# Kernel optimization log

Hardware: AMD Instinct MI355X
Metric: run time of the kernel (lower is better)

Reference implementation:

```python
import jax, jax.numpy as jnp
import numpy as np

B, LQ, LC, LN, D, H = 4, 1024, 1024, 1024, 1024, 16
HD = D // H
LS_INIT = 1e-4
RES_MAX = 10.0
EPS = 1e-5


def layernorm(x, g, b):
    mu = jnp.mean(x, axis=-1, keepdims=True)
    var = jnp.var(x, axis=-1, keepdims=True)
    return (x - mu) * jax.lax.rsqrt(var + EPS) * g + b


def setup_inputs() -> dict:
    key = jax.random.key(0)
    ks = jax.random.split(key, 12)
    s = 0.02
    return {
        "tight_tokens": jax.random.normal(ks[0], (B, LQ, D), jnp.float32),
        "context_tokens": jax.random.normal(ks[1], (B, LC, D), jnp.float32),
        "neighborhood_tokens": jax.random.normal(ks[2], (B, LN, D), jnp.float32),
        "ln_q_g": jnp.ones((D,), jnp.float32), "ln_q_b": jnp.zeros((D,), jnp.float32),
        "ln_kv_g": jnp.ones((D,), jnp.float32), "ln_kv_b": jnp.zeros((D,), jnp.float32),
        "in_proj_w": jax.random.normal(ks[3], (3 * D, D), jnp.float32) * s,
        "in_proj_b": jnp.zeros((3 * D,), jnp.float32),
        "out_proj_w": jax.random.normal(ks[4], (D, D), jnp.float32) * s,
        "out_proj_b": jnp.zeros((D,), jnp.float32),
        "cross_gamma": jnp.full((D,), LS_INIT, jnp.float32),
        "ln_f_g": jnp.ones((D,), jnp.float32), "ln_f_b": jnp.zeros((D,), jnp.float32),
        "w1": jax.random.normal(ks[5], (4 * D, D), jnp.float32) * s,
        "b1": jnp.zeros((4 * D,), jnp.float32),
        "w2": jax.random.normal(ks[6], (D, 4 * D), jnp.float32) * s,
        "b2": jnp.zeros((D,), jnp.float32),
        "ffn_gamma": jnp.full((D,), LS_INIT, jnp.float32),
    }


def reference(tight_tokens, context_tokens, neighborhood_tokens,
              ln_q_g, ln_q_b, ln_kv_g, ln_kv_b,
              in_proj_w, in_proj_b, out_proj_w, out_proj_b, cross_gamma,
              ln_f_g, ln_f_b, w1, b1, w2, b2, ffn_gamma):
    kv = jnp.concatenate([context_tokens, neighborhood_tokens], axis=1)  # [B, LKV, D]
    q_in = layernorm(tight_tokens, ln_q_g, ln_q_b)
    kv_in = layernorm(kv, ln_kv_g, ln_kv_b)

    wq, wk, wv = jnp.split(in_proj_w, 3, axis=0)
    bq, bk, bv = jnp.split(in_proj_b, 3, axis=0)
    q = (q_in @ wq.T + bq).reshape(B, LQ, H, HD)
    k = (kv_in @ wk.T + bk).reshape(B, -1, H, HD)
    v = (kv_in @ wv.T + bv).reshape(B, -1, H, HD)

    scores = jnp.einsum('bqhd,bkhd->bhqk', q, k) / jnp.sqrt(jnp.float32(HD))
    attn = jax.nn.softmax(scores, axis=-1)  # [B, H, LQ, LKV]
    ctx = jnp.einsum('bhqk,bkhd->bqhd', attn, v).reshape(B, LQ, D)
    attn_out = ctx @ out_proj_w.T + out_proj_b

    cg = jnp.clip(cross_gamma, -RES_MAX, RES_MAX)
    x = tight_tokens + attn_out * cg

    h = layernorm(x, ln_f_g, ln_f_b)
    h = jax.nn.gelu(h @ w1.T + b1, approximate=False) @ w2.T + b2
    fg = jnp.clip(ffn_gamma, -RES_MAX, RES_MAX)
    x = x + h * fg

    return x, attn.mean(axis=1)
```

## Files before the change

### kernel.cpp

```cpp
#include <hip/hip_runtime.h>
#include <math.h>

typedef unsigned short u16;
typedef __attribute__((ext_vector_type(8))) short bf16x8;
typedef __attribute__((ext_vector_type(4))) float f32x4;

#define MFMA16(a,b,c) __builtin_amdgcn_mfma_f32_16x16x32_bf16(a,b,c,0,0,0)

__device__ __forceinline__ u16 f2bf(float f){
  union { float f; unsigned int u; } x; x.f = f;
  unsigned int r = x.u + 0x7fffu + ((x.u >> 16) & 1u);
  return (u16)(r >> 16);
}

__device__ __forceinline__ void gload16(const void* g, void* lds){
  __builtin_amdgcn_global_load_lds(
    (const __attribute__((address_space(1))) unsigned int*)g,
    (__attribute__((address_space(3))) unsigned int*)lds, 16, 0, 0);
}

__global__ __launch_bounds__(256) void cvt_weights(
    const float* __restrict__ wqkv, const float* __restrict__ wo,
    const float* __restrict__ w1, const float* __restrict__ w2,
    u16* __restrict__ o0, u16* __restrict__ o1,
    u16* __restrict__ o2, u16* __restrict__ o3)
{
  int idx = blockIdx.x * 256 + threadIdx.x;
  const float* src; u16* dst;
  if (idx < 786432)                    { src = wqkv; dst = o0; }
  else if ((idx -= 786432) < 262144)   { src = wo;   dst = o1; }
  else if ((idx -= 262144) < 1048576)  { src = w1;   dst = o2; }
  else { idx -= 1048576;                 src = w2;   dst = o3; }
  float4 v = ((const float4*)src)[idx];
  short4 o;
  o.x = (short)f2bf(v.x); o.y = (short)f2bf(v.y);
  o.z = (short)f2bf(v.z); o.w = (short)f2bf(v.w);
  ((short4*)dst)[idx] = o;
}

template<int MODE>
__global__ __launch_bounds__(256) void ln_kernel(
    const float* __restrict__ s0, const float* __restrict__ s1,
    const float* __restrict__ g, const float* __restrict__ be,
    u16* __restrict__ out)
{
  int row = blockIdx.x, t = threadIdx.x;
  const float* src;
  if (MODE == 1) {
    int b = row >> 11, p = row & 2047;
    src = (p < 1024) ? s0 + ((long)(b*1024 + p))*1024
                     : s1 + ((long)(b*1024 + p - 1024))*1024;
  } else {
    src = s0 + (long)row * 1024;
  }
  float4 v = ((const float4*)src)[t];
  float s  = v.x + v.y + v.z + v.w;
  float ss = v.x*v.x + v.y*v.y + v.z*v.z + v.w*v.w;
  #pragma unroll
  for (int m = 1; m < 64; m <<= 1) { s += __shfl_xor(s, m); ss += __shfl_xor(ss, m); }
  __shared__ float red[8];
  int l = t & 63, w = t >> 6;
  if (l == 0) { red[w*2] = s; red[w*2+1] = ss; }
  __syncthreads();
  s  = red[0] + red[2] + red[4] + red[6];
  ss = red[1] + red[3] + red[5] + red[7];
  float mean = s * (1.0f/1024.0f);
  float var  = ss * (1.0f/1024.0f) - mean*mean;
  float rstd = rsqrtf(var + 1e-5f);
  float4 gv = ((const float4*)g)[t];
  float4 bv = ((const float4*)be)[t];
  short4 o;
  o.x = (short)f2bf((v.x-mean)*rstd*gv.x + bv.x);
  o.y = (short)f2bf((v.y-mean)*rstd*gv.y + bv.y);
  o.z = (short)f2bf((v.z-mean)*rstd*gv.z + bv.z);
  o.w = (short)f2bf((v.w-mean)*rstd*gv.w + bv.w);
  *(short4*)(out + (long)row*1024 + t*4) = o;
}

template<int EPI, int BM>
__global__ __launch_bounds__(256,2) void gemm_bt(
    const u16* __restrict__ A, const u16* __restrict__ Bt,
    int M, int N, int K,
    const float* __restrict__ bias,
    const float* __restrict__ gamma,
    const float* __restrict__ resid,
    float* __restrict__ outf,
    u16* __restrict__ outb0, u16* __restrict__ outb1)
{
  constexpr int MI = BM / 32;
  __shared__ __align__(16) u16 at[2][BM*64];
  __shared__ __align__(16) u16 bt[2][128*64];
  int nwg = gridDim.x;
  int bidx = (blockIdx.x & 7) * (nwg >> 3) + (blockIdx.x >> 3);
  int nb = N >> 7;
  int tm = bidx / nb, tn = bidx % nb;
  int m0 = tm * BM, n0 = tn << 7;
  int t = threadIdx.x, l = t & 63, w = t >> 6;
  int wr = (w >> 1) * (BM/2), wc = (w & 1) * 64;
  int fr = l & 15, fq = l >> 4;
  f32x4 acc[MI][4] = {};
  int rr = t >> 3;
  int cb = (t & 7) << 4;
  const char* Ab = (const char*)A;
  const char* Bp = (const char*)Bt;
  long ld = (long)K * 2;

#define G_STAGE(s, kt) do {                                                        \
    _Pragma("unroll")                                                              \
    for (int c = 0; c < MI; c++) {                                                 \
      int row = c*32 + rr;                                                         \
      gload16(Ab + (long)(m0 + row)*ld + (long)(kt)*2 + (cb ^ ((row & 7) << 4)),   \
              (char*)at[s] + c*4096 + w*1024);                                     \
    }                                                                              \
    _Pragma("unroll")                                                              \
    for (int c = 0; c < 4; c++) {                                                  \
      int row = c*32 + rr;                                                         \
      gload16(Bp + (long)(n0 + row)*ld + (long)(kt)*2 + (cb ^ ((row & 7) << 4)),   \
              (char*)bt[s] + c*4096 + w*1024);                                     \
    }                                                                              \
  } while (0)

  G_STAGE(0, 0);
  __syncthreads();
  int cur = 0;
  for (int kt = 0; kt < K; kt += 64) {
    if (kt + 64 < K) G_STAGE(cur ^ 1, kt + 64);
    #pragma unroll
    for (int ka = 0; ka < 2; ka++) {
      bf16x8 af[MI], bfv[4];
      #pragma unroll
      for (int i = 0; i < MI; i++) {
        int ra = wr + i*16 + fr;
        af[i] = *(const bf16x8*)((const char*)at[cur] + ra*128 + ((ka*64 + fq*16) ^ ((ra & 7) << 4)));
      }
      #pragma unroll
      for (int j = 0; j < 4; j++) {
        int rb = wc + j*16 + fr;
        bfv[j] = *(const bf16x8*)((const char*)bt[cur] + rb*128 + ((ka*64 + fq*16) ^ ((rb & 7) << 4)));
      }
      #pragma unroll
      for (int i = 0; i < MI; i++)
        #pragma unroll
        for (int j = 0; j < 4; j++)
          acc[i][j] = MFMA16(af[i], bfv[j], acc[i][j]);
    }
    __syncthreads();
    cur ^= 1;
  }
#undef G_STAGE
  #pragma unroll
  for (int i = 0; i < MI; i++) {
    #pragma unroll
    for (int j = 0; j < 4; j++) {
      #pragma unroll
      for (int r = 0; r < 4; r++) {
        int row = m0 + wr + i*16 + fq*4 + r;
        int col = n0 + wc + j*16 + fr;
        float v = acc[i][j][r];
        if constexpr (EPI == 0) {
          float qv = (v + bias[col]) * 0.18033688011112042f;
          int b = row >> 10, lq = row & 1023, h = col >> 6, hd = col & 63;
          outb0[(((long)(b*16 + h)) << 16) + (lq << 6) + hd] = f2bf(qv);
        } else if constexpr (EPI == 1) {
          float u = v + bias[col];
          int b = row >> 11, p = row & 2047;
          if (col < 1024) {
            int h = col >> 6, hd = col & 63;
            outb0[(((long)((b*16 + h)*2048 + p)) << 6) + hd] = f2bf(u);
          } else {
            int c2 = col - 1024, h = c2 >> 6, hd = c2 & 63;
            outb1[(((long)((b*16 + h)*64 + hd)) << 11) + p] = f2bf(u);
          }
        } else if constexpr (EPI == 2) {
          float gs = gamma[col]; gs = fminf(fmaxf(gs, -10.f), 10.f);
          long idx = (long)row*1024 + col;
          outf[idx] = resid[idx] + (v + bias[col]) * gs;
        } else if constexpr (EPI == 3) {
          float u = v + bias[col];
          float ge = 0.5f * u * (1.0f + erff(u * 0.70710678118654752f));
          outb0[(long)row*4096 + col] = f2bf(ge);
        } else {
          float gs = gamma[col]; gs = fminf(fmaxf(gs, -10.f), 10.f);
          long idx = (long)row*1024 + col;
          outf[idx] = resid[idx] + (v + bias[col]) * gs;
        }
      }
    }
  }
}

__global__ __launch_bounds__(256, 3) void flash_fwd(
    const u16* __restrict__ q, const u16* __restrict__ k,
    const u16* __restrict__ vt, u16* __restrict__ ctx,
    float* __restrict__ ilout)
{
  __shared__ __align__(16) u16 ks[2][64*64];
  __shared__ __align__(16) u16 vs[2][64*64];
  __shared__ __align__(16) char ps[4*4096];
  int nwg = gridDim.x;
  int bid = (blockIdx.x & 7) * (nwg >> 3) + (blockIdx.x >> 3);
  int qt = bid & 7, h = (bid >> 3) & 15, b = bid >> 7;
  int q0 = qt << 7;
  int t = threadIdx.x, l = t & 63, w = t >> 6;
  int fr = l & 15, fq = l >> 4;
  const char* qb = (const char*)(q  + (((long)(b*16 + h)) << 16));
  const char* kb = (const char*)(k  + (((long)(b*16 + h)) << 17));
  const char* vb = (const char*)(vt + (((long)(b*16 + h)) << 17));
  char* psw = ps + w*4096;
  int rr = t >> 3;
  int sc = (t & 7) << 4;

  #pragma unroll
  for (int c = 0; c < 2; c++) {
    int row = c*32 + rr;
    gload16(kb + (long)row*128 + (sc ^ ((row & 7) << 4)), (char*)ks[0] + c*4096 + w*1024);
    gload16(vb + (long)row*4096 + (sc ^ ((row & 7) << 4)), (char*)vs[0] + c*4096 + w*1024);
  }
  {
    int qr = l >> 3;
    #pragma unroll
    for (int c = 0; c < 4; c++) {
      int row = c*8 + qr;
      gload16(qb + (long)(q0 + w*32 + row)*128 + (sc ^ ((row & 7) << 4)), psw + c*1024);
    }
  }
  asm volatile("s_waitcnt vmcnt(0)" ::: "memory");
  bf16x8 qf[2][2];
  #pragma unroll
  for (int rf = 0; rf < 2; rf++) {
    int row = rf*16 + fr;
    qf[rf][0] = *(const bf16x8*)(psw + row*128 + ((fq*16) ^ ((row & 7) << 4)));
    qf[rf][1] = *(const bf16x8*)(psw + row*128 + ((64 + fq*16) ^ ((row & 7) << 4)));
  }
  asm volatile("s_waitcnt lgkmcnt(0)" ::: "memory");
  __builtin_amdgcn_s_barrier();
  asm volatile("" ::: "memory");

  f32x4 cacc[2][4] = {};
  f32x4 lrun[2] = {{0.f,0.f,0.f,0.f},{0.f,0.f,0.f,0.f}};
  int cur = 0;
  for (int kt = 0; kt < 2048; kt += 64) {
    int notlast = (kt + 64 < 2048);
    if (notlast) {
      #pragma unroll
      for (int c = 0; c < 2; c++) {
        int row = c*32 + rr;
        gload16(vb + (long)row*4096 + (long)(kt + 64)*2 + (sc ^ ((row & 7) << 4)),
                (char*)vs[cur ^ 1] + c*4096 + w*1024);
        gload16(kb + (long)(kt + 64 + row)*128 + (sc ^ ((row & 7) << 4)),
                (char*)ks[cur ^ 1] + c*4096 + w*1024);
      }
    }
    __builtin_amdgcn_sched_barrier(0);
    const char* ksb = (const char*)ks[cur];
    f32x4 sf[2][4];
    __builtin_amdgcn_s_setprio(1);
    #pragma unroll
    for (int cf = 0; cf < 4; cf++) {
      int row = cf*16 + fr;
      bf16x8 kf0 = *(const bf16x8*)(ksb + row*128 + ((fq*16) ^ ((row & 7) << 4)));
      bf16x8 kf1 = *(const bf16x8*)(ksb + row*128 + ((64 + fq*16) ^ ((row & 7) << 4)));
      #pragma unroll
      for (int rf = 0; rf < 2; rf++) {
        f32x4 a = {};
        a = MFMA16(qf[rf][0], kf0, a);
        sf[rf][cf] = MFMA16(qf[rf][1], kf1, a);
      }
    }
    __builtin_amdgcn_s_setprio(0);
    #pragma unroll
    for (int rf = 0; rf < 2; rf++)
      #pragma unroll
      for (int cf = 0; cf < 4; cf++)
        #pragma unroll
        for (int r = 0; r < 4; r++) {
          float pv = exp2f(sf[rf][cf][r]);
          lrun[rf][r] += pv;
          union { float f; unsigned int u; } pu; pu.f = pv;
          int prow = rf*16 + fq*4 + r;
          *(u16*)(psw + prow*128 + (((cf*16 + fr) << 1) ^ ((prow & 7) << 4))) = (u16)(pu.u >> 16);
        }
    bf16x8 pa[2][2];
    #pragma unroll
    for (int rf = 0; rf < 2; rf++) {
      int row = rf*16 + fr;
      pa[rf][0] = *(const bf16x8*)(psw + row*128 + ((fq*16) ^ ((row & 7) << 4)));
      pa[rf][1] = *(const bf16x8*)(psw + row*128 + ((64 + fq*16) ^ ((row & 7) << 4)));
    }
    __builtin_amdgcn_s_setprio(1);
    #pragma unroll
    for (int cfd = 0; cfd < 4; cfd++) {
      int hd = cfd*16 + fr;
      bf16x8 vf0 = *(const bf16x8*)((const char*)vs[cur] + hd*128 + ((fq*16) ^ ((hd & 7) << 4)));
      bf16x8 vf1 = *(const bf16x8*)((const char*)vs[cur] + hd*128 + ((64 + fq*16) ^ ((hd & 7) << 4)));
      #pragma unroll
      for (int rf = 0; rf < 2; rf++) {
        cacc[rf][cfd] = MFMA16(pa[rf][0], vf0, cacc[rf][cfd]);
        cacc[rf][cfd] = MFMA16(pa[rf][1], vf1, cacc[rf][cfd]);
      }
    }
    __builtin_amdgcn_s_setprio(0);
    if (notlast) {
      asm volatile("s_waitcnt vmcnt(0)" ::: "memory");
      __builtin_amdgcn_s_barrier();
      asm volatile("" ::: "memory");
    }
    cur ^= 1;
  }
  #pragma unroll
  for (int rf = 0; rf < 2; rf++) {
    float il4[4];
    #pragma unroll
    for (int r = 0; r < 4; r++) {
      float s = lrun[rf][r];
      #pragma unroll
      for (int msk = 1; msk < 16; msk <<= 1) s += __shfl_xor(s, msk, 16);
      il4[r] = 1.0f / s;
    }
    #pragma unroll
    for (int cf = 0; cf < 4; cf++)
      #pragma unroll
      for (int r = 0; r < 4; r++) {
        int row = q0 + w*32 + rf*16 + fq*4 + r;
        int col = h*64 + cf*16 + fr;
        ctx[(long)(b*1024 + row)*1024 + col] = f2bf(cacc[rf][cf][r] * il4[r]);
      }
    if (fr == 0) {
      #pragma unroll
      for (int r = 0; r < 4; r++) {
        int row = q0 + w*32 + rf*16 + fq*4 + r;
        long idx = (((long)(b*16 + h)) << 10) + row;
        ilout[idx] = il4[r];
      }
    }
  }
}

__global__ __launch_bounds__(256,2) void attn_mean(
    const u16* __restrict__ q, const u16* __restrict__ k,
    const float* __restrict__ il,
    float* __restrict__ out)
{
  __shared__ __align__(16) u16 qs[2][128*64];
  __shared__ __align__(16) u16 ks[2][128*64];
  __shared__ __align__(16) float ml[2][128];
  int nwg = gridDim.x;
  int bid = (blockIdx.x & 7) * (nwg >> 3) + (blockIdx.x >> 3);
  int kt = bid & 15, qt = (bid >> 4) & 7, b = bid >> 7;
  int q0 = qt << 7, k0 = kt << 7;
  int t = threadIdx.x, l = t & 63, w = t >> 6;
  int wr = (w >> 1) << 6, wc = (w & 1) << 6;
  int fr = l & 15, fq = l >> 4;
  int rr = t >> 3, cbb = (t & 7) << 4;
  const long bh = (long)b * 16;

#define AM_STAGE(hh, s) do {                                                        \
    const char* qb_ = (const char*)(q + ((bh + (hh)) << 16)) + (long)q0*128;        \
    const char* kb_ = (const char*)(k + ((bh + (hh)) << 17)) + (long)k0*128;        \
    _Pragma("unroll")                                                               \
    for (int c = 0; c < 4; c++) {                                                   \
      int row = c*32 + rr;                                                          \
      int sw = cbb ^ ((row & 7) << 4);                                              \
      gload16(qb_ + (long)row*128 + sw, (char*)qs[s] + c*4096 + w*1024);            \
      gload16(kb_ + (long)row*128 + sw, (char*)ks[s] + c*4096 + w*1024);            \
    }                                                                               \
    if (w == 0 && l < 32) {                                                         \
      gload16((const char*)(il + ((bh + (hh)) << 10) + q0) + l*16, (char*)ml[s]);   \
    }                                                                               \
  } while (0)

  AM_STAGE(0, 0);
  asm volatile("s_waitcnt vmcnt(0)" ::: "memory");
  __builtin_amdgcn_s_barrier();
  asm volatile("" ::: "memory");

  f32x4 macc[4][4] = {};
  for (int h = 0; h < 16; h++) {
    int cur = h & 1;
    if (h < 15) AM_STAGE(h + 1, cur ^ 1);
    const char* qsb = (const char*)qs[cur];
    const char* ksb = (const char*)ks[cur];
    const float* mlb = ml[cur];
    f32x4 ir4[4];
    #pragma unroll
    for (int i = 0; i < 4; i++)
      ir4[i] = *(const f32x4*)(mlb + wr + i*16 + fq*4);
    bf16x8 af[4][2], bf[4][2];
    #pragma unroll
    for (int i = 0; i < 4; i++) {
      int ra = wr + i*16 + fr;
      int rb = wc + i*16 + fr;
      af[i][0] = *(const bf16x8*)(qsb + ra*128 + ((fq*16) ^ ((ra & 7) << 4)));
      af[i][1] = *(const bf16x8*)(qsb + ra*128 + ((64 + fq*16) ^ ((ra & 7) << 4)));
      bf[i][0] = *(const bf16x8*)(ksb + rb*128 + ((fq*16) ^ ((rb & 7) << 4)));
      bf[i][1] = *(const bf16x8*)(ksb + rb*128 + ((64 + fq*16) ^ ((rb & 7) << 4)));
    }
    #pragma unroll
    for (int j = 0; j < 4; j++) {
      f32x4 sf[4];
      __builtin_amdgcn_s_setprio(1);
      #pragma unroll
      for (int i = 0; i < 4; i++) {
        f32x4 a = MFMA16(af[i][0], bf[j][0], {});
        sf[i] = MFMA16(af[i][1], bf[j][1], a);
      }
      __builtin_amdgcn_s_setprio(0);
      #pragma unroll
      for (int i = 0; i < 4; i++)
        #pragma unroll
        for (int r = 0; r < 4; r++)
          macc[i][j][r] += exp2f(sf[i][r]) * ir4[i][r];
    }
    asm volatile("s_waitcnt vmcnt(0)" ::: "memory");
    __builtin_amdgcn_s_barrier();
    asm volatile("" ::: "memory");
  }
#undef AM_STAGE
  #pragma unroll
  for (int i = 0; i < 4; i++)
    #pragma unroll
    for (int j = 0; j < 4; j++)
      #pragma unroll
      for (int r = 0; r < 4; r++) {
        int row = q0 + wr + i*16 + fq*4 + r;
        int col = k0 + wc + j*16 + fr;
        out[((long)(b*1024 + row) << 11) + col] = macc[i][j][r] * 0.0625f;
      }
}

extern "C" void kernel_launch(void* const* d_in, const int* in_sizes, int n_in,
                              void* d_out, int out_size, void* d_ws, size_t ws_size,
                              hipStream_t stream)
{
  (void)in_sizes; (void)n_in; (void)out_size; (void)ws_size;
  const float* tight = (const float*)d_in[0];
  const float* ctxt  = (const float*)d_in[1];
  const float* nbh   = (const float*)d_in[2];
  const float* lnqg  = (const float*)d_in[3];
  const float* lnqb  = (const float*)d_in[4];
  const float* lnkg  = (const float*)d_in[5];
  const float* lnkb  = (const float*)d_in[6];
  const float* wqkv  = (const float*)d_in[7];
  const float* bqkv  = (const float*)d_in[8];
  const float* wo    = (const float*)d_in[9];
  const float* bo    = (const float*)d_in[10];
  const float* cg    = (const float*)d_in[11];
  const float* lnfg  = (const float*)d_in[12];
  const float* lnfb  = (const float*)d_in[13];
  const float* w1    = (const float*)d_in[14];
  const float* b1    = (const float*)d_in[15];
  const float* w2    = (const float*)d_in[16];
  const float* b2    = (const float*)d_in[17];
  const float* fg    = (const float*)d_in[18];

  char* p = (char*)d_ws;
  u16* wqkv_bf = (u16*)p; p += 3072L*1024*2;
  u16* wo_bf   = (u16*)p; p += 1024L*1024*2;
  u16* w1_bf   = (u16*)p; p += 4096L*1024*2;
  u16* w2_bf   = (u16*)p; p += 1024L*4096*2;
  u16* qin_bf  = (u16*)p; p += 4096L*1024*2;
  u16* kvin_bf = (u16*)p; p += 8192L*1024*2;
  u16* q_bf    = (u16*)p; p += 4L*16*1024*64*2;
  u16* k_bf    = (u16*)p; p += 4L*16*2048*64*2;
  u16* vt_bf   = (u16*)p; p += 4L*16*64*2048*2;
  u16* ctx_bf  = (u16*)p; p += 4096L*1024*2;
  float* il_f  = (float*)p; p += 4L*16*1024*4;
  float* x_f   = (float*)p; p += 4096L*1024*4;
  u16* hln_bf  = (u16*)p; p += 4096L*1024*2;
  u16* gelu_bf = (u16*)p; p += 4096L*4096*2;

  float* x_out    = (float*)d_out;
  float* mean_out = x_out + 4194304;

  cvt_weights<<<12288, 256, 0, stream>>>(wqkv, wo, w1, w2, wqkv_bf, wo_bf, w1_bf, w2_bf);
  ln_kernel<0><<<4096, 256, 0, stream>>>(tight, nullptr, lnqg, lnqb, qin_bf);
  ln_kernel<1><<<8192, 256, 0, stream>>>(ctxt, nbh, lnkg, lnkb, kvin_bf);
  gemm_bt<0,64><<<512, 256, 0, stream>>>(qin_bf, wqkv_bf, 4096, 1024, 1024,
                                      bqkv, nullptr, nullptr, nullptr, q_bf, nullptr);
  gemm_bt<1,128><<<1024, 256, 0, stream>>>(kvin_bf, wqkv_bf + 1024L*1024, 8192, 2048, 1024,
                                       bqkv + 1024, nullptr, nullptr, nullptr, k_bf, vt_bf);
  flash_fwd<<<512, 256, 0, stream>>>(q_bf, k_bf, vt_bf, ctx_bf, il_f);
  attn_mean<<<512, 256, 0, stream>>>(q_bf, k_bf, il_f, mean_out);
  gemm_bt<2,64><<<512, 256, 0, stream>>>(ctx_bf, wo_bf, 4096, 1024, 1024,
                                      bo, cg, tight, x_f, nullptr, nullptr);
  ln_kernel<0><<<4096, 256, 0, stream>>>(x_f, nullptr, lnfg, lnfb, hln_bf);
  gemm_bt<3,128><<<1024, 256, 0, stream>>>(hln_bf, w1_bf, 4096, 4096, 1024,
                                       b1, nullptr, nullptr, nullptr, gelu_bf, nullptr);
  gemm_bt<4,64><<<512, 256, 0, stream>>>(gelu_bf, w2_bf, 4096, 1024, 4096,
                                      b2, fg, x_f, x_out, nullptr, nullptr);
}
```

Baseline: 371.7 us.

## Add 256x256-tile 8-wave GEMM with phased pipelining for KV and FFN1

```diff
diff --git a/kernel.cpp b/kernel.cpp
--- a/kernel.cpp
+++ b/kernel.cpp
@@ -161,16 +161,6 @@
           float qv = (v + bias[col]) * 0.18033688011112042f;
           int b = row >> 10, lq = row & 1023, h = col >> 6, hd = col & 63;
           outb0[(((long)(b*16 + h)) << 16) + (lq << 6) + hd] = f2bf(qv);
-        } else if constexpr (EPI == 1) {
-          float u = v + bias[col];
-          int b = row >> 11, p = row & 2047;
-          if (col < 1024) {
-            int h = col >> 6, hd = col & 63;
-            outb0[(((long)((b*16 + h)*2048 + p)) << 6) + hd] = f2bf(u);
-          } else {
-            int c2 = col - 1024, h = c2 >> 6, hd = c2 & 63;
-            outb1[(((long)((b*16 + h)*64 + hd)) << 11) + p] = f2bf(u);
-          }
         } else if constexpr (EPI == 2) {
           float gs = gamma[col]; gs = fminf(fmaxf(gs, -10.f), 10.f);
           long idx = (long)row*1024 + col;
@@ -183,6 +173,158 @@
           float gs = gamma[col]; gs = fminf(fmaxf(gs, -10.f), 10.f);
           long idx = (long)row*1024 + col;
           outf[idx] = resid[idx] + (v + bias[col]) * gs;
+        }
+      }
+    }
+  }
+}
+
+template<int EPI>
+__global__ __launch_bounds__(512, 2) void gemm256(
+    const u16* __restrict__ A, const u16* __restrict__ Bt,
+    int M, int N, int K,
+    const float* __restrict__ bias,
+    u16* __restrict__ outb0, u16* __restrict__ outb1)
+{
+  __shared__ __align__(16) u16 As[2][256*64];
+  __shared__ __align__(16) u16 Bs[2][256*64];
+  int nwg = gridDim.x;
+  int bidx = (blockIdx.x & 7) * (nwg >> 3) + (blockIdx.x >> 3);
+  int nb = N >> 8;
+  int tm = bidx / nb, tn = bidx % nb;
+  int m0 = tm << 8, n0 = tn << 8;
+  int t = threadIdx.x, l = t & 63, w = t >> 6;
+  int wm = w >> 2, wn = w & 3;
+  int fr = l & 15, fq = l >> 4;
+  int sr = t >> 3;
+  int scb = (t & 7) << 4;
+  int s7 = (sr & 7) << 4;
+  const char* Ab = (const char*)A;
+  const char* Bp = (const char*)Bt;
+  long ld = (long)K * 2;
+
+#define STAGE_AQ(slot, kt, q) do {                                               \
+    int grow = (sr < 32) ? ((q)*32 + sr) : (128 + (q)*32 + sr - 32);             \
+    int abase = (w < 4) ? ((q)*32 + w*8) : (128 + (q)*32 + (w - 4)*8);           \
+    gload16(Ab + (long)(m0 + grow)*ld + (long)(kt)*2 + (scb ^ s7),               \
+            (char*)As[slot] + abase*128);                                        \
+  } while (0)
+#define STAGE_BH(slot, kt, h) do {                                               \
+    int r0 = (h)*128 + sr;                                                       \
+    gload16(Bp + (long)(n0 + r0)*ld + (long)(kt)*2 + (scb ^ s7),                 \
+            (char*)Bs[slot] + ((h)*128 + w*8)*128);                              \
+    gload16(Bp + (long)(n0 + r0 + 64)*ld + (long)(kt)*2 + (scb ^ s7),            \
+            (char*)Bs[slot] + ((h)*128 + 64 + w*8)*128);                         \
+  } while (0)
+
+  f32x4 acc[8][4] = {};
+  int NT = K >> 6;
+
+  STAGE_BH(0, 0, 0); STAGE_BH(0, 0, 1);
+  STAGE_AQ(0, 0, 0); STAGE_AQ(0, 0, 1); STAGE_AQ(0, 0, 2); STAGE_AQ(0, 0, 3);
+  STAGE_BH(1, 64, 0); STAGE_BH(1, 64, 1);
+  asm volatile("s_waitcnt vmcnt(4)" ::: "memory");
+  __builtin_amdgcn_s_barrier();
+  asm volatile("" ::: "memory");
+
+#define MFMA_PHASE(mibase)                                                       \
+    __builtin_amdgcn_s_setprio(1);                                               \
+    _Pragma("unroll")                                                            \
+    for (int nj = 0; nj < 4; nj++) {                                             \
+      acc[(mibase)][nj]   = MFMA16(a00, bfr[nj][0], acc[(mibase)][nj]);          \
+      acc[(mibase)][nj]   = MFMA16(a01, bfr[nj][1], acc[(mibase)][nj]);          \
+      acc[(mibase)+1][nj] = MFMA16(a10, bfr[nj][0], acc[(mibase)+1][nj]);        \
+      acc[(mibase)+1][nj] = MFMA16(a11, bfr[nj][1], acc[(mibase)+1][nj]);        \
+    }                                                                            \
+    __builtin_amdgcn_s_setprio(0);
+
+#define READ_A(p)                                                                \
+    int r0_ = wm*128 + (2*(p))*16 + fr;                                          \
+    int r1_ = r0_ + 16;                                                          \
+    bf16x8 a00 = *(const bf16x8*)(Ab_s + r0_*128 + ((fq*16) ^ ((r0_ & 7) << 4)));        \
+    bf16x8 a01 = *(const bf16x8*)(Ab_s + r0_*128 + ((64 + fq*16) ^ ((r0_ & 7) << 4)));   \
+    bf16x8 a10 = *(const bf16x8*)(Ab_s + r1_*128 + ((fq*16) ^ ((r1_ & 7) << 4)));        \
+    bf16x8 a11 = *(const bf16x8*)(Ab_s + r1_*128 + ((64 + fq*16) ^ ((r1_ & 7) << 4)));
+
+  for (int tt = 0; tt < NT; tt++) {
+    int s = tt & 1;
+    const char* Ab_s = (const char*)As[s];
+    const char* Bb_s = (const char*)Bs[s];
+    int kt1 = (tt + 1) << 6, kt2 = (tt + 2) << 6;
+    bf16x8 bfr[4][2];
+    {
+      #pragma unroll
+      for (int nj = 0; nj < 4; nj++) {
+        int rb = wn*64 + nj*16 + fr;
+        bfr[nj][0] = *(const bf16x8*)(Bb_s + rb*128 + ((fq*16) ^ ((rb & 7) << 4)));
+        bfr[nj][1] = *(const bf16x8*)(Bb_s + rb*128 + ((64 + fq*16) ^ ((rb & 7) << 4)));
+      }
+      READ_A(0)
+      if (tt + 1 < NT) { STAGE_AQ(s ^ 1, kt1, 0); STAGE_AQ(s ^ 1, kt1, 1); }
+      asm volatile("s_waitcnt lgkmcnt(8)" ::: "memory");
+      __builtin_amdgcn_s_barrier();
+      asm volatile("s_waitcnt lgkmcnt(0)" ::: "memory");
+      MFMA_PHASE(0)
+      __builtin_amdgcn_s_barrier();
+    }
+    {
+      READ_A(1)
+      if (tt + 1 < NT) { STAGE_AQ(s ^ 1, kt1, 2); STAGE_AQ(s ^ 1, kt1, 3); }
+      __builtin_amdgcn_s_barrier();
+      asm volatile("s_waitcnt lgkmcnt(0)" ::: "memory");
+      MFMA_PHASE(2)
+      __builtin_amdgcn_s_barrier();
+    }
+    {
+      READ_A(2)
+      if (tt + 2 < NT) STAGE_BH(s, kt2, 0);
+      __builtin_amdgcn_s_barrier();
+      asm volatile("s_waitcnt lgkmcnt(0)" ::: "memory");
+      MFMA_PHASE(4)
+      __builtin_amdgcn_s_barrier();
+    }
+    {
+      READ_A(3)
+      if (tt + 2 < NT) STAGE_BH(s, kt2, 1);
+      __builtin_amdgcn_s_barrier();
+      asm volatile("s_waitcnt lgkmcnt(0)" ::: "memory");
+      MFMA_PHASE(6)
+      if (tt + 1 < NT) {
+        if (tt + 2 < NT) { asm volatile("s_waitcnt vmcnt(4)" ::: "memory"); }
+        else             { asm volatile("s_waitcnt vmcnt(0)" ::: "memory"); }
+      }
+      __builtin_amdgcn_s_barrier();
+      asm volatile("" ::: "memory");
+    }
+  }
+#undef READ_A
+#undef MFMA_PHASE
+#undef STAGE_AQ
+#undef STAGE_BH
+
+  #pragma unroll
+  for (int mi = 0; mi < 8; mi++) {
+    #pragma unroll
+    for (int nj = 0; nj < 4; nj++) {
+      #pragma unroll
+      for (int r = 0; r < 4; r++) {
+        int row = m0 + wm*128 + mi*16 + fq*4 + r;
+        int col = n0 + wn*64 + nj*16 + fr;
+        float v = acc[mi][nj][r];
+        if constexpr (EPI == 1) {
+          float u = v + bias[col];
+          int b = row >> 11, p = row & 2047;
+          if (col < 1024) {
+            int h = col >> 6, hd = col & 63;
+            outb0[(((long)((b*16 + h)*2048 + p)) << 6) + hd] = f2bf(u);
+          } else {
+            int c2 = col - 1024, h = c2 >> 6, hd = c2 & 63;
+            outb1[(((long)((b*16 + h)*64 + hd)) << 11) + p] = f2bf(u);
+          }
+        } else {
+          float u = v + bias[col];
+          float ge = 0.5f * u * (1.0f + erff(u * 0.70710678118654752f));
+          outb0[(long)row*4096 + col] = f2bf(ge);
         }
       }
     }
@@ -477,15 +619,15 @@
   ln_kernel<1><<<8192, 256, 0, stream>>>(ctxt, nbh, lnkg, lnkb, kvin_bf);
   gemm_bt<0,64><<<512, 256, 0, stream>>>(qin_bf, wqkv_bf, 4096, 1024, 1024,
                                       bqkv, nullptr, nullptr, nullptr, q_bf, nullptr);
-  gemm_bt<1,128><<<1024, 256, 0, stream>>>(kvin_bf, wqkv_bf + 1024L*1024, 8192, 2048, 1024,
-                                       bqkv + 1024, nullptr, nullptr, nullptr, k_bf, vt_bf);
+  gemm256<1><<<256, 512, 0, stream>>>(kvin_bf, wqkv_bf + 1024L*1024, 8192, 2048, 1024,
+                                      bqkv + 1024, k_bf, vt_bf);
   flash_fwd<<<512, 256, 0, stream>>>(q_bf, k_bf, vt_bf, ctx_bf, il_f);
   attn_mean<<<512, 256, 0, stream>>>(q_bf, k_bf, il_f, mean_out);
   gemm_bt<2,64><<<512, 256, 0, stream>>>(ctx_bf, wo_bf, 4096, 1024, 1024,
                                       bo, cg, tight, x_f, nullptr, nullptr);
   ln_kernel<0><<<4096, 256, 0, stream>>>(x_f, nullptr, lnfg, lnfb, hln_bf);
-  gemm_bt<3,128><<<1024, 256, 0, stream>>>(hln_bf, w1_bf, 4096, 4096, 1024,
-                                       b1, nullptr, nullptr, nullptr, gelu_bf, nullptr);
+  gemm256<3><<<256, 512, 0, stream>>>(hln_bf, w1_bf, 4096, 4096, 1024,
+                                      b1, gelu_bf, nullptr);
   gemm_bt<4,64><<<512, 256, 0, stream>>>(gelu_bf, w2_bf, 4096, 1024, 4096,
                                       b2, fg, x_f, x_out, nullptr, nullptr);
 }
```

After: 360.6 us. 3.0% less time.
